# Performance work log

Hardware: AMD Instinct MI355X
Metric: run time of the kernel (lower is better)

## Reference

```python
import jax, jax.numpy as jnp
import numpy as np

B, L, C_IN, D, H, DFF, NL, NC, PH = 32, 512, 16, 512, 8, 2048, 3, 10, 128
DH = D // H


def circ_conv1d(x, w):
    # x: [B, C, S] with circular padding 1 on spatial dim, w: [O, C, 3]
    xp = jnp.concatenate([x[..., -1:], x, x[..., :1]], axis=-1)
    return jax.lax.conv_general_dilated(xp, w, (1,), 'VALID',
                                        dimension_numbers=('NCH', 'OIH', 'NCH'))


def positional_embedding(length, d):
    pos = jnp.arange(length, dtype=jnp.float32)[:, None]
    div = jnp.exp(jnp.arange(0, d, 2, dtype=jnp.float32) * (-np.log(10000.0) / d))
    pe = jnp.zeros((length, d), jnp.float32)
    pe = pe.at[:, 0::2].set(jnp.sin(pos * div))
    pe = pe.at[:, 1::2].set(jnp.cos(pos * div))
    return pe


def layer_norm(x, g, b):
    m = jnp.mean(x, -1, keepdims=True)
    v = jnp.var(x, -1, keepdims=True)
    return (x - m) / jnp.sqrt(v + 1e-5) * g + b


def projector(x, stats, conv_w, w0, b0, w1, b1, w2):
    # x: [B, L, C_IN] (channels = seq_len, spatial = enc_in), stats: [B, 1, C_IN]
    y = circ_conv1d(x, conv_w)                     # [B, 1, C_IN]
    y = jnp.concatenate([y, stats], axis=1)        # [B, 2, C_IN]
    y = y.reshape(x.shape[0], -1)                  # [B, 2*C_IN]
    h = jax.nn.relu(y @ w0.T + b0)
    h = jax.nn.relu(h @ w1.T + b1)
    return h @ w2.T                                # no bias on output


def setup_inputs() -> dict:
    key = jax.random.key(0)
    ks = iter(jax.random.split(key, 64))
    rn = lambda shape, s=0.02: jax.random.normal(next(ks), shape, jnp.float32) * s
    inp = {
        'x_enc': jax.random.normal(next(ks), (B, L, C_IN), jnp.float32),
        'x_mark_enc': jnp.ones((B, L), jnp.float32),
        'tok_w': rn((D, C_IN, 3)),
        'Wq': rn((NL, D, D)), 'bq': jnp.zeros((NL, D)),
        'Wk': rn((NL, D, D)), 'bk': jnp.zeros((NL, D)),
        'Wv': rn((NL, D, D)), 'bv': jnp.zeros((NL, D)),
        'Wo': rn((NL, D, D)), 'bo': jnp.zeros((NL, D)),
        'W1': rn((NL, DFF, D)), 'b1': jnp.zeros((NL, DFF)),
        'W2': rn((NL, D, DFF)), 'b2': jnp.zeros((NL, D)),
        'ln1_g': jnp.ones((NL, D)), 'ln1_b': jnp.zeros((NL, D)),
        'ln2_g': jnp.ones((NL, D)), 'ln2_b': jnp.zeros((NL, D)),
        'norm_g': jnp.ones((D,)), 'norm_b': jnp.zeros((D,)),
        'proj_w': rn((NC, D * L)), 'proj_b': jnp.zeros((NC,)),
        'tau_conv_w': rn((1, L, 3)), 'tau_w0': rn((PH, 2 * C_IN)), 'tau_b0': jnp.zeros((PH,)),
        'tau_w1': rn((PH, PH)), 'tau_b1': jnp.zeros((PH,)), 'tau_w2': rn((1, PH)),
        'del_conv_w': rn((1, L, 3)), 'del_w0': rn((PH, 2 * C_IN)), 'del_b0': jnp.zeros((PH,)),
        'del_w1': rn((PH, PH)), 'del_b1': jnp.zeros((PH,)), 'del_w2': rn((L, PH)),
    }
    return inp


def reference(x_enc, x_mark_enc, tok_w,
              Wq, bq, Wk, bk, Wv, bv, Wo, bo,
              W1, b1, W2, b2, ln1_g, ln1_b, ln2_g, ln2_b,
              norm_g, norm_b, proj_w, proj_b,
              tau_conv_w, tau_w0, tau_b0, tau_w1, tau_b1, tau_w2,
              del_conv_w, del_w0, del_b0, del_w1, del_b1, del_w2):
    # De-stationary statistics (detached in the original)
    x_raw = jax.lax.stop_gradient(x_enc)
    mean_enc = jnp.mean(x_raw, 1, keepdims=True)                 # [B,1,C]
    std_enc = jnp.sqrt(jnp.var(x_raw, 1, keepdims=True) + 1e-5)  # [B,1,C]
    tau = jnp.exp(projector(x_raw, std_enc, tau_conv_w, tau_w0, tau_b0,
                            tau_w1, tau_b1, tau_w2))             # [B,1]
    delta = projector(x_raw, mean_enc, del_conv_w, del_w0, del_b0,
                      del_w1, del_b1, del_w2)                    # [B,L]

    # DataEmbedding: circular token conv + sinusoidal positional encoding
    tok = circ_conv1d(jnp.transpose(x_enc, (0, 2, 1)), tok_w)    # [B,D,L]
    x = jnp.transpose(tok, (0, 2, 1)) + positional_embedding(L, D)[None]

    scale = 1.0 / np.sqrt(DH)
    tau4 = tau.reshape(B, 1, 1, 1)
    delta4 = delta[:, None, None, :]
    for i in range(NL):
        q = (x @ Wq[i].T + bq[i]).reshape(B, L, H, DH)
        k = (x @ Wk[i].T + bk[i]).reshape(B, L, H, DH)
        v = (x @ Wv[i].T + bv[i]).reshape(B, L, H, DH)
        scores = jnp.einsum('blhe,bshe->bhls', q, k) * tau4 + delta4
        A = jax.nn.softmax(scale * scores, axis=-1)
        o = jnp.einsum('bhls,bshd->blhd', A, v).reshape(B, L, D)
        o = o @ Wo[i].T + bo[i]
        x = layer_norm(x + o, ln1_g[i], ln1_b[i])
        y = jax.nn.gelu(x @ W1[i].T + b1[i], approximate=False) @ W2[i].T + b2[i]
        x = layer_norm(x + y, ln2_g[i], ln2_b[i])
    x = layer_norm(x, norm_g, norm_b)

    out = jax.nn.gelu(x, approximate=False)
    out = out * x_mark_enc[..., None]
    out = out.reshape(B, -1) @ proj_w.T + proj_b                 # [B, NC]
    return out
```

## Files before the change

kernel.cpp:

```cpp
#include <hip/hip_runtime.h>
#include <hip/hip_bf16.h>
#include <cstdint>

#define DEVINL __device__ __forceinline__

typedef unsigned short u16;
typedef short bf16x8 __attribute__((ext_vector_type(8)));
typedef float f32x4 __attribute__((ext_vector_type(4)));

DEVINL u16 f2b(float f) {
    union { float f; uint32_t u; } x{f};
    uint32_t r = x.u + 0x7fffu + ((x.u >> 16) & 1u);
    return (u16)(r >> 16);
}
DEVINL float b2f(u16 h) {
    union { uint32_t u; float f; } x{(uint32_t)h << 16};
    return x.f;
}
DEVINL float gelu_exact(float v) {
    return 0.5f * v * (1.0f + erff(v * 0.70710678118654752f));
}
DEVINL void gload_lds16(const void* g, void* l) {
    __builtin_amdgcn_global_load_lds(
        (const __attribute__((address_space(1))) void*)(uintptr_t)g,
        (__attribute__((address_space(3))) void*)(uint32_t)(uintptr_t)l,
        16, 0, 0);
}

__global__ void f2b_kernel(const float* __restrict__ in, u16* __restrict__ out, int n) {
    int i = (blockIdx.x * 256 + threadIdx.x) * 8;
    if (i + 8 <= n) {
        float4 a = *(const float4*)(in + i);
        float4 b = *(const float4*)(in + i + 4);
        u16 t[8] = {f2b(a.x), f2b(a.y), f2b(a.z), f2b(a.w),
                    f2b(b.x), f2b(b.y), f2b(b.z), f2b(b.w)};
        *(uint4*)(out + i) = *(const uint4*)t;
    }
}

__global__ void packb_kernel(const float* __restrict__ bq, const float* __restrict__ bk,
                             const float* __restrict__ bv, float* __restrict__ out) {
    int idx = blockIdx.x * 256 + threadIdx.x;
    if (idx >= 3 * 1536) return;
    int i = idx / 1536, j = idx - i * 1536;
    float v = (j < 512) ? bq[i * 512 + j]
            : (j < 1024) ? bk[i * 512 + j - 512]
                         : bv[i * 512 + j - 1024];
    out[idx] = v;
}

__global__ void pe_kernel(float* __restrict__ pet) {
    int l = blockIdx.x, d2 = threadIdx.x;
    float freq = expf(-(float)(2 * d2) * 0.0179889460390f);
    float ang = (float)l * freq;
    pet[l * 512 + 2 * d2]     = sinf(ang);
    pet[l * 512 + 2 * d2 + 1] = cosf(ang);
}

__global__ void stats_kernel(const float* __restrict__ xe, float* __restrict__ mean,
                             float* __restrict__ stdv) {
    int b = blockIdx.x, ln = threadIdx.x;
    int c = ln & 15, part = ln >> 4;
    float s = 0.f, sq = 0.f;
    for (int l = part; l < 512; l += 4) {
        float x = xe[(size_t)b * 8192 + l * 16 + c];
        s += x; sq += x * x;
    }
    s += __shfl_xor(s, 16);  s += __shfl_xor(s, 32);
    sq += __shfl_xor(sq, 16); sq += __shfl_xor(sq, 32);
    if (part == 0) {
        float m = s * (1.0f / 512.0f);
        mean[b * 16 + c] = m;
        stdv[b * 16 + c] = sqrtf(sq * (1.0f / 512.0f) - m * m + 1e-5f);
    }
}

__global__ __launch_bounds__(128)
void proj_kernel(const float* __restrict__ xe, const float* __restrict__ stats,
                 const float* __restrict__ cw, const float* __restrict__ w0,
                 const float* __restrict__ b0, const float* __restrict__ w1,
                 const float* __restrict__ b1, const float* __restrict__ w2,
                 float* __restrict__ outp, int outn, int do_exp) {
    __shared__ float zl[32], h0l[128], h1l[128], red[2];
    int b = blockIdx.x, tid = threadIdx.x;
    {
        int c = tid >> 3, part = tid & 7;
        float acc = 0.f;
        for (int l = part; l < 512; l += 8) {
            const float* xr = xe + (size_t)b * 8192 + l * 16;
            float w0v = cw[l * 3 + 0], w1v = cw[l * 3 + 1], w2v = cw[l * 3 + 2];
            acc += xr[(c + 15) & 15] * w0v + xr[c] * w1v + xr[(c + 1) & 15] * w2v;
        }
        acc += __shfl_xor(acc, 1); acc += __shfl_xor(acc, 2); acc += __shfl_xor(acc, 4);
        if (part == 0) zl[c] = acc;
        if (tid < 16) zl[16 + tid] = stats[b * 16 + tid];
    }
    __syncthreads();
    {
        float acc = b0[tid];
        #pragma unroll
        for (int i = 0; i < 32; ++i) acc += zl[i] * w0[tid * 32 + i];
        h0l[tid] = fmaxf(acc, 0.0f);
    }
    __syncthreads();
    {
        float acc = b1[tid];
        for (int i = 0; i < 128; ++i) acc += h0l[i] * w1[tid * 128 + i];
        h1l[tid] = fmaxf(acc, 0.0f);
    }
    __syncthreads();
    if (outn == 1) {
        float p = h1l[tid] * w2[tid];
        p += __shfl_xor(p, 1);  p += __shfl_xor(p, 2);  p += __shfl_xor(p, 4);
        p += __shfl_xor(p, 8);  p += __shfl_xor(p, 16); p += __shfl_xor(p, 32);
        if ((tid & 63) == 0) red[tid >> 6] = p;
        __syncthreads();
        if (tid == 0) {
            float v = red[0] + red[1];
            outp[b] = do_exp ? expf(v) : v;
        }
    } else {
        for (int l = tid; l < outn; l += 128) {
            float acc = 0.f;
            for (int i = 0; i < 128; ++i) acc += h1l[i] * w2[l * 128 + i];
            outp[(size_t)b * outn + l] = acc;
        }
    }
}

__global__ __launch_bounds__(256)
void tokconv_kernel(const float* __restrict__ xe, const float* __restrict__ tw,
                    const float* __restrict__ pet,
                    float* __restrict__ xf, u16* __restrict__ xb) {
    __shared__ float xs[34][16];
    int lt = blockIdx.x, b = blockIdx.y, tid = threadIdx.x;
    int l0 = lt * 32;
    for (int idx = tid; idx < 34 * 16; idx += 256) {
        int r = idx >> 4, c = idx & 15;
        int gl = (l0 - 1 + r + 512) & 511;
        xs[r][c] = xe[(size_t)b * 8192 + gl * 16 + c];
    }
    __syncthreads();
    for (int dd = tid; dd < 512; dd += 256) {
        float twr[48];
        #pragma unroll
        for (int i = 0; i < 48; ++i) twr[i] = tw[dd * 48 + i];
        for (int l = 0; l < 32; ++l) {
            float acc = 0.f;
            #pragma unroll
            for (int c = 0; c < 16; ++c) {
                acc += xs[l][c]     * twr[c * 3 + 0];
                acc += xs[l + 1][c] * twr[c * 3 + 1];
                acc += xs[l + 2][c] * twr[c * 3 + 2];
            }
            float vv = acc + pet[(size_t)(l0 + l) * 512 + dd];
            size_t idx = ((size_t)b * 512 + l0 + l) * 512 + dd;
            xf[idx] = vv;
            xb[idx] = f2b(vv);
        }
    }
}

template <int ACT, int OBF>
__global__ __launch_bounds__(256)
void gemm_bt(const u16* __restrict__ A, const u16* __restrict__ B,
             const float* __restrict__ bias, void* __restrict__ Cv,
             int M, int N, int K) {
    __shared__ u16 smem[2][2][128 * 32];
    const int tid = threadIdx.x, wv = tid >> 6, ln = tid & 63;
    const int m0 = blockIdx.y * 128, n0 = blockIdx.x * 128;
    const int wm = (wv >> 1) * 64, wn = (wv & 1) * 64;
    const int lo = ln & 15, hi = ln >> 4;
    f32x4 acc[4][4] = {};
    const int r0 = wv * 16 + (ln >> 2);
    const int sl = ln & 3;

    auto stage = [&](int buf, int kt) {
        #pragma unroll
        for (int c = 0; c < 2; ++c) {
            int row = r0 + c * 64;
            int ssl = sl ^ ((row >> 1) & 3);
            int ldsoff = row * 32 + sl * 8;
            gload_lds16(A + (size_t)(m0 + row) * K + kt + ssl * 8, (char*)smem[buf][0] + ldsoff * 2);
            gload_lds16(B + (size_t)(n0 + row) * K + kt + ssl * 8, (char*)smem[buf][1] + ldsoff * 2);
        }
    };

    stage(0, 0);
    __syncthreads();
    int cur = 0;
    const int nt = K >> 5;
    for (int t = 0; t < nt; ++t) {
        if (t + 1 < nt) stage(cur ^ 1, (t + 1) * 32);
        bf16x8 af[4], bfr[4];
        #pragma unroll
        for (int i = 0; i < 4; ++i) {
            int row = wm + i * 16 + lo;
            int slot = hi ^ ((row >> 1) & 3);
            af[i] = *(const bf16x8*)(smem[cur][0] + row * 32 + slot * 8);
        }
        #pragma unroll
        for (int j = 0; j < 4; ++j) {
            int row = wn + j * 16 + lo;
            int slot = hi ^ ((row >> 1) & 3);
            bfr[j] = *(const bf16x8*)(smem[cur][1] + row * 32 + slot * 8);
        }
        #pragma unroll
        for (int i = 0; i < 4; ++i)
            #pragma unroll
            for (int j = 0; j < 4; ++j)
                acc[i][j] = __builtin_amdgcn_mfma_f32_16x16x32_bf16(af[i], bfr[j], acc[i][j], 0, 0, 0);
        __syncthreads();
        cur ^= 1;
    }

    float* ep = (float*)smem + wv * (16 * 68);
    #pragma unroll
    for (int i = 0; i < 4; ++i) {
        #pragma unroll
        for (int j = 0; j < 4; ++j) {
            int col = n0 + wn + j * 16 + lo;
            float bv = bias[col];
            #pragma unroll
            for (int r = 0; r < 4; ++r) {
                float v = acc[i][j][r] + bv;
                if (ACT == 1) v = gelu_exact(v);
                ep[(hi * 4 + r) * 68 + j * 16 + lo] = v;
            }
        }
        #pragma unroll
        for (int pp = 0; pp < 4; ++pp) {
            int rl = pp * 4 + hi;
            float4 vv = *(const float4*)(ep + rl * 68 + lo * 4);
            size_t row = (size_t)(m0 + wm + i * 16 + rl);
            int col = n0 + wn + lo * 4;
            if (OBF) {
                u16 t4[4] = {f2b(vv.x), f2b(vv.y), f2b(vv.z), f2b(vv.w)};
                *(uint2*)((u16*)Cv + row * N + col) = *(const uint2*)t4;
            } else {
                *(float4*)((float*)Cv + row * N + col) = vv;
            }
        }
    }
}

__global__ __launch_bounds__(512)
void attn2_kernel(const u16* __restrict__ qkv, const float* __restrict__ tau,
                  const float* __restrict__ delta, u16* __restrict__ o) {
    __shared__ u16 KL[64 * 64];
    __shared__ u16 VT[64 * 72];
    __shared__ u16 PL[8][32 * 64];
    const int tid = threadIdx.x, w = tid >> 6, ln = tid & 63;
    const int lo = ln & 15, hi = ln >> 4;
    const int qh = blockIdx.x, h = blockIdx.y, b = blockIdx.z;
    const size_t qrow0 = (size_t)b * 512;
    const u16* qp = qkv;
    const u16* kp = qkv + 512;
    const u16* vp = qkv + 1024;
    const int hofs = h * 64;
    const float ts = tau[b] * 0.125f;
    u16* Pw = (u16*)PL[w];
    const int q0 = qh * 256 + w * 32;

    bf16x8 qa[2][2];
    #pragma unroll
    for (int i = 0; i < 2; ++i)
        #pragma unroll
        for (int ks = 0; ks < 2; ++ks)
            qa[i][ks] = *(const bf16x8*)(qp + (qrow0 + q0 + i * 16 + lo) * 1536 + hofs + ks * 32 + hi * 8);

    float m_run[2] = {-1e30f, -1e30f};
    float l_run[2] = {0.f, 0.f};
    f32x4 oacc[2][4] = {};

    const int vsl = tid & 7, vsr = tid >> 3;
    uint4 vreg = *(const uint4*)(vp + (qrow0 + vsr) * 1536 + hofs + vsl * 8);

    for (int nt = 0; nt < 8; ++nt) {
        __syncthreads();
        {
            int s = tid >> 3, j = tid & 7;
            int jl = j ^ (s & 7);
            gload_lds16(kp + (qrow0 + nt * 64 + s) * 1536 + hofs + jl * 8,
                        (char*)KL + tid * 16);
        }
        {
            u16 tmp[8]; *(uint4*)tmp = vreg;
            #pragma unroll
            for (int e = 0; e < 8; ++e) {
                int d = vsl * 8 + e;
                int byt = d * 144 + (((vsr >> 3) ^ vsl) << 4) + (vsr & 7) * 2;
                *(u16*)((char*)VT + byt) = tmp[e];
            }
        }
        if (nt < 7)
            vreg = *(const uint4*)(vp + (qrow0 + (nt + 1) * 64 + vsr) * 1536 + hofs + vsl * 8);
        __syncthreads();

        f32x4 sacc[2][4] = {};
        #pragma unroll
        for (int ks = 0; ks < 2; ++ks) {
            #pragma unroll
            for (int jn = 0; jn < 4; ++jn) {
                int s = jn * 16 + lo;
                int phys = (ks * 4 + hi) ^ (s & 7);
                bf16x8 kb = *(const bf16x8*)((const char*)KL + s * 128 + phys * 16);
                #pragma unroll
                for (int i = 0; i < 2; ++i)
                    sacc[i][jn] = __builtin_amdgcn_mfma_f32_16x16x32_bf16(kb, qa[i][ks], sacc[i][jn], 0, 0, 0);
            }
        }
        float tmax[2] = {-1e30f, -1e30f};
        #pragma unroll
        for (int jn = 0; jn < 4; ++jn) {
            float4 dv4 = *(const float4*)(delta + b * 512 + nt * 64 + jn * 16 + hi * 4);
            float dv[4] = {dv4.x, dv4.y, dv4.z, dv4.w};
            #pragma unroll
            for (int i = 0; i < 2; ++i)
                #pragma unroll
                for (int r = 0; r < 4; ++r) {
                    float v = sacc[i][jn][r] * ts + dv[r] * 0.125f;
                    sacc[i][jn][r] = v;
                    tmax[i] = fmaxf(tmax[i], v);
                }
        }
        #pragma unroll
        for (int i = 0; i < 2; ++i) {
            tmax[i] = fmaxf(tmax[i], __shfl_xor(tmax[i], 16));
            tmax[i] = fmaxf(tmax[i], __shfl_xor(tmax[i], 32));
            float mnew = fmaxf(m_run[i], tmax[i]);
            float fac = __expf(m_run[i] - mnew);
            m_run[i] = mnew;
            l_run[i] *= fac;
            #pragma unroll
            for (int jd = 0; jd < 4; ++jd)
                #pragma unroll
                for (int r = 0; r < 4; ++r) oacc[i][jd][r] *= fac;
        }
        #pragma unroll
        for (int i = 0; i < 2; ++i) {
            float ls = 0.f;
            #pragma unroll
            for (int jn = 0; jn < 4; ++jn) {
                float p0 = __expf(sacc[i][jn][0] - m_run[i]);
                float p1 = __expf(sacc[i][jn][1] - m_run[i]);
                float p2 = __expf(sacc[i][jn][2] - m_run[i]);
                float p3 = __expf(sacc[i][jn][3] - m_run[i]);
                ls += (p0 + p1) + (p2 + p3);
                uint2 pk;
                pk.x = (uint32_t)f2b(p0) | ((uint32_t)f2b(p1) << 16);
                pk.y = (uint32_t)f2b(p2) | ((uint32_t)f2b(p3) << 16);
                int q = i * 16 + lo;
                int ls16 = jn * 2 + (hi >> 1);
                int byt = q * 128 + (((ls16 ^ (q & 7)) << 4)) + (hi & 1) * 8;
                *(uint2*)((char*)Pw + byt) = pk;
            }
            ls += __shfl_xor(ls, 16);
            ls += __shfl_xor(ls, 32);
            l_run[i] += ls;
        }
        #pragma unroll
        for (int ks2 = 0; ks2 < 2; ++ks2) {
            bf16x8 pa[2];
            #pragma unroll
            for (int i = 0; i < 2; ++i) {
                int q = i * 16 + lo;
                int phys = (ks2 * 4 + hi) ^ (q & 7);
                pa[i] = *(const bf16x8*)((const char*)Pw + q * 128 + phys * 16);
            }
            #pragma unroll
            for (int jd = 0; jd < 4; ++jd) {
                int d = jd * 16 + lo;
                int cs = (ks2 * 4 + hi) ^ ((d >> 3) & 7);
                bf16x8 vb = *(const bf16x8*)((const char*)VT + d * 144 + cs * 16);
                #pragma unroll
                for (int i = 0; i < 2; ++i)
                    oacc[i][jd] = __builtin_amdgcn_mfma_f32_16x16x32_bf16(vb, pa[i], oacc[i][jd], 0, 0, 0);
            }
        }
    }
    #pragma unroll
    for (int i = 0; i < 2; ++i) {
        float inv = 1.0f / l_run[i];
        #pragma unroll
        for (int jd = 0; jd < 4; ++jd) {
            u16 t4[4];
            #pragma unroll
            for (int r = 0; r < 4; ++r) t4[r] = f2b(oacc[i][jd][r] * inv);
            size_t row = qrow0 + q0 + i * 16 + lo;
            *(uint2*)(o + row * 512 + hofs + jd * 16 + hi * 4) = *(const uint2*)t4;
        }
    }
}

__global__ __launch_bounds__(256)
void ln_kernel(const float* __restrict__ xin, const float* __restrict__ res,
               const float* __restrict__ g, const float* __restrict__ bta,
               float* __restrict__ xout, u16* __restrict__ xbf) {
    const int row = blockIdx.x * 4 + (threadIdx.x >> 6);
    const int ln = threadIdx.x & 63;
    const float* xr = xin + (size_t)row * 512;
    const float* rr = res + (size_t)row * 512;
    float4 a = *(const float4*)(xr + ln * 4);
    float4 c = *(const float4*)(xr + 256 + ln * 4);
    float4 ra = *(const float4*)(rr + ln * 4);
    float4 rc = *(const float4*)(rr + 256 + ln * 4);
    a.x += ra.x; a.y += ra.y; a.z += ra.z; a.w += ra.w;
    c.x += rc.x; c.y += rc.y; c.z += rc.z; c.w += rc.w;
    float s = a.x + a.y + a.z + a.w + c.x + c.y + c.z + c.w;
    float sq = a.x*a.x + a.y*a.y + a.z*a.z + a.w*a.w + c.x*c.x + c.y*c.y + c.z*c.z + c.w*c.w;
    #pragma unroll
    for (int m = 1; m < 64; m <<= 1) { s += __shfl_xor(s, m); sq += __shfl_xor(sq, m); }
    float mean = s * 0.001953125f;
    float var = sq * 0.001953125f - mean * mean;
    float rstd = rsqrtf(var + 1e-5f);
    float4 g0 = *(const float4*)(g + ln * 4);
    float4 g1 = *(const float4*)(g + 256 + ln * 4);
    float4 b0 = *(const float4*)(bta + ln * 4);
    float4 b1 = *(const float4*)(bta + 256 + ln * 4);
    float4 o0, o1;
    o0.x = (a.x - mean) * rstd * g0.x + b0.x;
    o0.y = (a.y - mean) * rstd * g0.y + b0.y;
    o0.z = (a.z - mean) * rstd * g0.z + b0.z;
    o0.w = (a.w - mean) * rstd * g0.w + b0.w;
    o1.x = (c.x - mean) * rstd * g1.x + b1.x;
    o1.y = (c.y - mean) * rstd * g1.y + b1.y;
    o1.z = (c.z - mean) * rstd * g1.z + b1.z;
    o1.w = (c.w - mean) * rstd * g1.w + b1.w;
    *(float4*)(xout + (size_t)row * 512 + ln * 4) = o0;
    *(float4*)(xout + (size_t)row * 512 + 256 + ln * 4) = o1;
    u16 t0[4] = {f2b(o0.x), f2b(o0.y), f2b(o0.z), f2b(o0.w)};
    u16 t1[4] = {f2b(o1.x), f2b(o1.y), f2b(o1.z), f2b(o1.w)};
    *(uint2*)(xbf + (size_t)row * 512 + ln * 4) = *(const uint2*)t0;
    *(uint2*)(xbf + (size_t)row * 512 + 256 + ln * 4) = *(const uint2*)t1;
}

__global__ __launch_bounds__(256)
void lngelu_kernel(const float* __restrict__ xin, const float* __restrict__ g,
                   const float* __restrict__ bta, const float* __restrict__ mark,
                   u16* __restrict__ outb) {
    const int row = blockIdx.x * 4 + (threadIdx.x >> 6);
    const int ln = threadIdx.x & 63;
    const float* xr = xin + (size_t)row * 512;
    float4 a = *(const float4*)(xr + ln * 4);
    float4 c = *(const float4*)(xr + 256 + ln * 4);
    float s = a.x + a.y + a.z + a.w + c.x + c.y + c.z + c.w;
    float sq = a.x*a.x + a.y*a.y + a.z*a.z + a.w*a.w + c.x*c.x + c.y*c.y + c.z*c.z + c.w*c.w;
    #pragma unroll
    for (int m = 1; m < 64; m <<= 1) { s += __shfl_xor(s, m); sq += __shfl_xor(sq, m); }
    float mean = s * 0.001953125f;
    float var = sq * 0.001953125f - mean * mean;
    float rstd = rsqrtf(var + 1e-5f);
    float mk = mark[row];
    float4 g0 = *(const float4*)(g + ln * 4);
    float4 g1 = *(const float4*)(g + 256 + ln * 4);
    float4 b0 = *(const float4*)(bta + ln * 4);
    float4 b1 = *(const float4*)(bta + 256 + ln * 4);
    float v0 = gelu_exact((a.x - mean) * rstd * g0.x + b0.x) * mk;
    float v1 = gelu_exact((a.y - mean) * rstd * g0.y + b0.y) * mk;
    float v2 = gelu_exact((a.z - mean) * rstd * g0.z + b0.z) * mk;
    float v3 = gelu_exact((a.w - mean) * rstd * g0.w + b0.w) * mk;
    float v4 = gelu_exact((c.x - mean) * rstd * g1.x + b1.x) * mk;
    float v5 = gelu_exact((c.y - mean) * rstd * g1.y + b1.y) * mk;
    float v6 = gelu_exact((c.z - mean) * rstd * g1.z + b1.z) * mk;
    float v7 = gelu_exact((c.w - mean) * rstd * g1.w + b1.w) * mk;
    u16 t0[4] = {f2b(v0), f2b(v1), f2b(v2), f2b(v3)};
    u16 t1[4] = {f2b(v4), f2b(v5), f2b(v6), f2b(v7)};
    *(uint2*)(outb + (size_t)row * 512 + ln * 4) = *(const uint2*)t0;
    *(uint2*)(outb + (size_t)row * 512 + 256 + ln * 4) = *(const uint2*)t1;
}

__global__ __launch_bounds__(256)
void fproj_kernel(const u16* __restrict__ gb, const u16* __restrict__ pw,
                  const float* __restrict__ pb, float* __restrict__ out) {
    __shared__ float red[32][4];
    int n = blockIdx.x, ks = blockIdx.y, tid = threadIdx.x;
    float acc[32];
    #pragma unroll
    for (int m = 0; m < 32; ++m) acc[m] = 0.f;
    for (int j = 0; j < 8; ++j) {
        size_t k0 = (size_t)ks * 16384 + j * 2048 + tid * 8;
        bf16x8 w8 = *(const bf16x8*)(pw + (size_t)n * 262144 + k0);
        float wf[8];
        #pragma unroll
        for (int e = 0; e < 8; ++e) wf[e] = b2f((u16)w8[e]);
        #pragma unroll
        for (int m = 0; m < 32; ++m) {
            bf16x8 g8 = *(const bf16x8*)(gb + (size_t)m * 262144 + k0);
            float a = acc[m];
            #pragma unroll
            for (int e = 0; e < 8; ++e) a += b2f((u16)g8[e]) * wf[e];
            acc[m] = a;
        }
    }
    int w = tid >> 6;
    #pragma unroll
    for (int m = 0; m < 32; ++m) {
        float s = acc[m];
        s += __shfl_xor(s, 1);  s += __shfl_xor(s, 2);  s += __shfl_xor(s, 4);
        s += __shfl_xor(s, 8);  s += __shfl_xor(s, 16); s += __shfl_xor(s, 32);
        if ((tid & 63) == 0) red[m][w] = s;
    }
    __syncthreads();
    if (tid < 32) {
        int m = tid;
        float s = red[m][0] + red[m][1] + red[m][2] + red[m][3];
        if (ks == 0) s += pb[n];
        atomicAdd(&out[m * 10 + n], s);
    }
}

extern "C" void kernel_launch(void* const* d_in, const int* in_sizes, int n_in,
                              void* d_out, int out_size, void* d_ws, size_t ws_size,
                              hipStream_t stream) {
    const float* x_enc  = (const float*)d_in[0];
    const float* x_mark = (const float*)d_in[1];
    const float* tok_w  = (const float*)d_in[2];
    const float* Wq = (const float*)d_in[3];   const float* bq = (const float*)d_in[4];
    const float* Wk = (const float*)d_in[5];   const float* bk = (const float*)d_in[6];
    const float* Wv = (const float*)d_in[7];   const float* bv = (const float*)d_in[8];
    const float* Wo = (const float*)d_in[9];   const float* bo = (const float*)d_in[10];
    const float* W1 = (const float*)d_in[11];  const float* b1 = (const float*)d_in[12];
    const float* W2 = (const float*)d_in[13];  const float* b2 = (const float*)d_in[14];
    const float* ln1_g = (const float*)d_in[15]; const float* ln1_b = (const float*)d_in[16];
    const float* ln2_g = (const float*)d_in[17]; const float* ln2_b = (const float*)d_in[18];
    const float* norm_g = (const float*)d_in[19]; const float* norm_b = (const float*)d_in[20];
    const float* proj_w = (const float*)d_in[21]; const float* proj_b = (const float*)d_in[22];
    const float* tau_cw = (const float*)d_in[23];
    const float* tau_w0 = (const float*)d_in[24]; const float* tau_b0 = (const float*)d_in[25];
    const float* tau_w1 = (const float*)d_in[26]; const float* tau_b1 = (const float*)d_in[27];
    const float* tau_w2 = (const float*)d_in[28];
    const float* del_cw = (const float*)d_in[29];
    const float* del_w0 = (const float*)d_in[30]; const float* del_b0 = (const float*)d_in[31];
    const float* del_w1 = (const float*)d_in[32]; const float* del_b1 = (const float*)d_in[33];
    const float* del_w2 = (const float*)d_in[34];
    float* out = (float*)d_out;

    char* ws = (char*)d_ws;
    size_t off = 0;
    auto alloc = [&](size_t bytes) -> void* {
        void* p = ws + off;
        off += (bytes + 255) & ~(size_t)255;
        return p;
    };
    u16* wqkvb = (u16*)alloc((size_t)3 * 786432 * 2);
    u16* wob = (u16*)alloc(786432 * 2);
    u16* w1b = (u16*)alloc(3145728 * 2);
    u16* w2b = (u16*)alloc(3145728 * 2);
    u16* pwb = (u16*)alloc(2621440 * 2);
    float* bqkvb = (float*)alloc(3 * 1536 * 4);
    float* petab = (float*)alloc((size_t)262144 * 4);
    float* meanb = (float*)alloc(512 * 4);
    float* stdb  = (float*)alloc(512 * 4);
    float* taub  = (float*)alloc(32 * 4);
    float* delb  = (float*)alloc(16384 * 4);
    float* xf = (float*)alloc((size_t)8388608 * 4);
    u16*  xb  = (u16*)alloc((size_t)8388608 * 2);
    float* sf = (float*)alloc((size_t)8388608 * 4);
    u16* qkvb = (u16*)alloc((size_t)16384 * 1536 * 2);
    u16* ob   = (u16*)alloc((size_t)8388608 * 2);
    u16* hb   = qkvb;
    u16* gbuf = qkvb;

    auto cvt = [&](const float* src, u16* dst, int n) {
        f2b_kernel<<<dim3((n + 2047) / 2048), dim3(256), 0, stream>>>(src, dst, n);
    };
    for (int i = 0; i < 3; ++i) {
        cvt(Wq + (size_t)i * 262144, wqkvb + (size_t)i * 786432 + 0,      262144);
        cvt(Wk + (size_t)i * 262144, wqkvb + (size_t)i * 786432 + 262144, 262144);
        cvt(Wv + (size_t)i * 262144, wqkvb + (size_t)i * 786432 + 524288, 262144);
    }
    cvt(Wo, wob, 786432);
    cvt(W1, w1b, 3145728); cvt(W2, w2b, 3145728);
    cvt(proj_w, pwb, 2621440);
    packb_kernel<<<dim3(18), dim3(256), 0, stream>>>(bq, bk, bv, bqkvb);
    pe_kernel<<<dim3(512), dim3(256), 0, stream>>>(petab);

    stats_kernel<<<dim3(32), dim3(64), 0, stream>>>(x_enc, meanb, stdb);
    proj_kernel<<<dim3(32), dim3(128), 0, stream>>>(x_enc, stdb, tau_cw, tau_w0, tau_b0,
                                                    tau_w1, tau_b1, tau_w2, taub, 1, 1);
    proj_kernel<<<dim3(32), dim3(128), 0, stream>>>(x_enc, meanb, del_cw, del_w0, del_b0,
                                                    del_w1, del_b1, del_w2, delb, 512, 0);
    tokconv_kernel<<<dim3(16, 32), dim3(256), 0, stream>>>(x_enc, tok_w, petab, xf, xb);

    for (int i = 0; i < 3; ++i) {
        const u16* wqkv_i = wqkvb + (size_t)i * 786432;
        const u16* wo_i = wob + (size_t)i * 262144;
        const u16* w1_i = w1b + (size_t)i * 1048576;
        const u16* w2_i = w2b + (size_t)i * 1048576;
        gemm_bt<0, 1><<<dim3(12, 128), dim3(256), 0, stream>>>(xb, wqkv_i, bqkvb + i * 1536, qkvb, 16384, 1536, 512);
        attn2_kernel<<<dim3(2, 8, 32), dim3(512), 0, stream>>>(qkvb, taub, delb, ob);
        gemm_bt<0, 0><<<dim3(4, 128), dim3(256), 0, stream>>>(ob, wo_i, bo + i * 512, sf, 16384, 512, 512);
        ln_kernel<<<dim3(4096), dim3(256), 0, stream>>>(xf, sf, ln1_g + i * 512, ln1_b + i * 512, xf, xb);
        gemm_bt<1, 1><<<dim3(16, 128), dim3(256), 0, stream>>>(xb, w1_i, b1 + i * 2048, hb, 16384, 2048, 512);
        gemm_bt<0, 0><<<dim3(4, 128), dim3(256), 0, stream>>>(hb, w2_i, b2 + i * 512, sf, 16384, 512, 2048);
        ln_kernel<<<dim3(4096), dim3(256), 0, stream>>>(xf, sf, ln2_g + i * 512, ln2_b + i * 512, xf, xb);
    }

    lngelu_kernel<<<dim3(4096), dim3(256), 0, stream>>>(xf, norm_g, norm_b, x_mark, gbuf);
    hipMemsetAsync(d_out, 0, (size_t)out_size * 4, stream);
    fproj_kernel<<<dim3(10, 16), dim3(256), 0, stream>>>(gbuf, pwb, proj_b, out);
}
```

Baseline: 967.2 us.

## Split-K the N=512 GEMMs into two halves, merging partials in layernorm

The Wo and W2 GEMMs (N=512, which gave only 512 blocks) now launch with a grid z-dimension of 2. Each z-slice covers half of K. The first slice writes fp32 output with bias, and the second writes a bf16 partial sum with no bias into a scratch buffer. The layernorm kernel now reads both partials plus the residual and sums them, so GPU occupancy doubles for these GEMMs. The cost is extra traffic for the partial buffers and a loss of precision, because one partial is rounded to bf16.

Measured after the change: 1.075 ms. 11.1% more time.

```diff
diff --git a/kernel.cpp b/kernel.cpp
--- a/kernel.cpp
+++ b/kernel.cpp
@@ -164,16 +164,18 @@
 template <int ACT, int OBF>
 __global__ __launch_bounds__(256)
 void gemm_bt(const u16* __restrict__ A, const u16* __restrict__ B,
-             const float* __restrict__ bias, void* __restrict__ Cv,
-             int M, int N, int K) {
+             const float* __restrict__ bias, void* __restrict__ Cv0,
+             u16* __restrict__ Cv1, int M, int N, int K, int Kc) {
     __shared__ u16 smem[2][2][128 * 32];
     const int tid = threadIdx.x, wv = tid >> 6, ln = tid & 63;
     const int m0 = blockIdx.y * 128, n0 = blockIdx.x * 128;
+    const int kz = blockIdx.z;
     const int wm = (wv >> 1) * 64, wn = (wv & 1) * 64;
     const int lo = ln & 15, hi = ln >> 4;
     f32x4 acc[4][4] = {};
     const int r0 = wv * 16 + (ln >> 2);
     const int sl = ln & 3;
+    const int k0 = kz * Kc;
 
     auto stage = [&](int buf, int kt) {
         #pragma unroll
@@ -186,12 +188,12 @@
         }
     };
 
-    stage(0, 0);
+    stage(0, k0);
     __syncthreads();
     int cur = 0;
-    const int nt = K >> 5;
+    const int nt = Kc >> 5;
     for (int t = 0; t < nt; ++t) {
-        if (t + 1 < nt) stage(cur ^ 1, (t + 1) * 32);
+        if (t + 1 < nt) stage(cur ^ 1, k0 + (t + 1) * 32);
         bf16x8 af[4], bfr[4];
         #pragma unroll
         for (int i = 0; i < 4; ++i) {
@@ -214,17 +216,18 @@
         cur ^= 1;
     }
 
+    const bool second = (kz != 0);
     float* ep = (float*)smem + wv * (16 * 68);
     #pragma unroll
     for (int i = 0; i < 4; ++i) {
         #pragma unroll
         for (int j = 0; j < 4; ++j) {
             int col = n0 + wn + j * 16 + lo;
-            float bv = bias[col];
+            float bv = second ? 0.0f : bias[col];
             #pragma unroll
             for (int r = 0; r < 4; ++r) {
                 float v = acc[i][j][r] + bv;
-                if (ACT == 1) v = gelu_exact(v);
+                if (ACT == 1 && !second) v = gelu_exact(v);
                 ep[(hi * 4 + r) * 68 + j * 16 + lo] = v;
             }
         }
@@ -234,11 +237,14 @@
             float4 vv = *(const float4*)(ep + rl * 68 + lo * 4);
             size_t row = (size_t)(m0 + wm + i * 16 + rl);
             int col = n0 + wn + lo * 4;
-            if (OBF) {
+            if (second) {
                 u16 t4[4] = {f2b(vv.x), f2b(vv.y), f2b(vv.z), f2b(vv.w)};
-                *(uint2*)((u16*)Cv + row * N + col) = *(const uint2*)t4;
+                *(uint2*)(Cv1 + row * N + col) = *(const uint2*)t4;
+            } else if (OBF) {
+                u16 t4[4] = {f2b(vv.x), f2b(vv.y), f2b(vv.z), f2b(vv.w)};
+                *(uint2*)((u16*)Cv0 + row * N + col) = *(const uint2*)t4;
             } else {
-                *(float4*)((float*)Cv + row * N + col) = vv;
+                *(float4*)((float*)Cv0 + row * N + col) = vv;
             }
         }
     }
@@ -394,19 +400,27 @@
 }
 
 __global__ __launch_bounds__(256)
-void ln_kernel(const float* __restrict__ xin, const float* __restrict__ res,
-               const float* __restrict__ g, const float* __restrict__ bta,
-               float* __restrict__ xout, u16* __restrict__ xbf) {
+void ln3_kernel(const float* __restrict__ xin, const float* __restrict__ res0,
+                const u16* res1, const float* __restrict__ g,
+                const float* __restrict__ bta,
+                float* __restrict__ xout, u16* xbf) {
     const int row = blockIdx.x * 4 + (threadIdx.x >> 6);
     const int ln = threadIdx.x & 63;
     const float* xr = xin + (size_t)row * 512;
-    const float* rr = res + (size_t)row * 512;
+    const float* rr = res0 + (size_t)row * 512;
+    const u16* pr = res1 + (size_t)row * 512;
     float4 a = *(const float4*)(xr + ln * 4);
     float4 c = *(const float4*)(xr + 256 + ln * 4);
     float4 ra = *(const float4*)(rr + ln * 4);
     float4 rc = *(const float4*)(rr + 256 + ln * 4);
-    a.x += ra.x; a.y += ra.y; a.z += ra.z; a.w += ra.w;
-    c.x += rc.x; c.y += rc.y; c.z += rc.z; c.w += rc.w;
+    uint2 pa_ = *(const uint2*)(pr + ln * 4);
+    uint2 pc_ = *(const uint2*)(pr + 256 + ln * 4);
+    const u16* pa16 = (const u16*)&pa_;
+    const u16* pc16 = (const u16*)&pc_;
+    a.x += ra.x + b2f(pa16[0]); a.y += ra.y + b2f(pa16[1]);
+    a.z += ra.z + b2f(pa16[2]); a.w += ra.w + b2f(pa16[3]);
+    c.x += rc.x + b2f(pc16[0]); c.y += rc.y + b2f(pc16[1]);
+    c.z += rc.z + b2f(pc16[2]); c.w += rc.w + b2f(pc16[3]);
     float s = a.x + a.y + a.z + a.w + c.x + c.y + c.z + c.w;
     float sq = a.x*a.x + a.y*a.y + a.z*a.z + a.w*a.w + c.x*c.x + c.y*c.y + c.z*c.z + c.w*c.w;
     #pragma unroll
@@ -561,6 +575,8 @@
     u16* ob   = (u16*)alloc((size_t)8388608 * 2);
     u16* hb   = qkvb;
     u16* gbuf = qkvb;
+    u16* p1o  = qkvb;
+    u16* p1f  = xb;
 
     auto cvt = [&](const float* src, u16* dst, int n) {
         f2b_kernel<<<dim3((n + 2047) / 2048), dim3(256), 0, stream>>>(src, dst, n);
@@ -588,13 +604,19 @@
         const u16* wo_i = wob + (size_t)i * 262144;
         const u16* w1_i = w1b + (size_t)i * 1048576;
         const u16* w2_i = w2b + (size_t)i * 1048576;
-        gemm_bt<0, 1><<<dim3(12, 128), dim3(256), 0, stream>>>(xb, wqkv_i, bqkvb + i * 1536, qkvb, 16384, 1536, 512);
+        gemm_bt<0, 1><<<dim3(12, 128, 1), dim3(256), 0, stream>>>(
+            xb, wqkv_i, bqkvb + i * 1536, qkvb, nullptr, 16384, 1536, 512, 512);
         attn2_kernel<<<dim3(2, 8, 32), dim3(512), 0, stream>>>(qkvb, taub, delb, ob);
-        gemm_bt<0, 0><<<dim3(4, 128), dim3(256), 0, stream>>>(ob, wo_i, bo + i * 512, sf, 16384, 512, 512);
-        ln_kernel<<<dim3(4096), dim3(256), 0, stream>>>(xf, sf, ln1_g + i * 512, ln1_b + i * 512, xf, xb);
-        gemm_bt<1, 1><<<dim3(16, 128), dim3(256), 0, stream>>>(xb, w1_i, b1 + i * 2048, hb, 16384, 2048, 512);
-        gemm_bt<0, 0><<<dim3(4, 128), dim3(256), 0, stream>>>(hb, w2_i, b2 + i * 512, sf, 16384, 512, 2048);
-        ln_kernel<<<dim3(4096), dim3(256), 0, stream>>>(xf, sf, ln2_g + i * 512, ln2_b + i * 512, xf, xb);
+        gemm_bt<0, 0><<<dim3(4, 128, 2), dim3(256), 0, stream>>>(
+            ob, wo_i, bo + i * 512, sf, p1o, 16384, 512, 512, 256);
+        ln3_kernel<<<dim3(4096), dim3(256), 0, stream>>>(xf, sf, p1o,
+            ln1_g + i * 512, ln1_b + i * 512, xf, xb);
+        gemm_bt<1, 1><<<dim3(16, 128, 1), dim3(256), 0, stream>>>(
+            xb, w1_i, b1 + i * 2048, hb, nullptr, 16384, 2048, 512, 512);
+        gemm_bt<0, 0><<<dim3(4, 128, 2), dim3(256), 0, stream>>>(
+            hb, w2_i, b2 + i * 512, sf, p1f, 16384, 512, 2048, 1024);
+        ln3_kernel<<<dim3(4096), dim3(256), 0, stream>>>(xf, sf, p1f,
+            ln2_g + i * 512, ln2_b + i * 512, xf, xb);
     }
 
     lngelu_kernel<<<dim3(4096), dim3(256), 0, stream>>>(xf, norm_g, norm_b, x_mark, gbuf);
```
